# Performance work log

Measured on AMD Instinct MI355X. Metric: run time of the kernel, lower is better.

The kernel has to match this reference:

```python
import jax, jax.numpy as jnp
import numpy as np

B, SECL, WORDL = 16, 8, 512
S = SECL * WORDL
H, E, V, NOOV = 256, 128, 50000, 32
EOS = 3
FSIZE = 2  # config.mode == 'train'


def setup_inputs() -> dict:
    key = jax.random.key(0)
    ks = jax.random.split(key, 24)
    g = lambda i, shape, s=0.02: jax.random.normal(ks[i], shape, jnp.float32) * s
    inp = jax.random.randint(ks[0], (B,), 0, V)
    inp = inp.at[:4].set(EOS)  # exercise focus-update branch
    h = g(1, (B, H), 0.1)
    c = g(2, (B, H), 0.1)
    enc_outputs = g(3, (B, S, 2 * H), 1.0)
    enc_feature = g(4, (B, S, 2 * H), 0.1)
    enc_sec_output = g(5, (B, SECL, 2 * H), 1.0)
    enc_mask = jnp.ones((B, S), jnp.float32)
    sec_mask = jnp.ones((B, SECL), jnp.float32)
    prev_context = g(6, (B, 2 * H), 0.1)
    zeros_oov = jnp.zeros((B, NOOV), jnp.float32)
    enc_input_oov = jax.random.randint(ks[7], (B, S), 0, V + NOOV)
    coverage = jnp.zeros((B, S), jnp.float32)
    # sparse nonneg focus distribution over sections (guaranteed >=1 nonzero/row)
    u = jax.random.uniform(ks[8], (B, SECL))
    f = u * (u > 0.5)
    fb = jax.nn.one_hot(jnp.argmax(u, axis=1), SECL)
    f = jnp.where(f.sum(1, keepdims=True) > 0, f, fb)
    focus = f / f.sum(1, keepdims=True)
    params = dict(
        embedding=g(9, (V, E)),
        W_comb=g(10, (E, 2 * H + E)), b_comb=jnp.zeros((E,), jnp.float32),
        W_ih=g(11, (4 * H, E)), W_hh=g(12, (4 * H, H)),
        b_ih=jnp.zeros((4 * H,), jnp.float32), b_hh=jnp.zeros((4 * H,), jnp.float32),
        W_d=g(13, (2 * H, 2 * H)), b_d=jnp.zeros((2 * H,), jnp.float32),
        W_feat=g(14, (2 * H, 2 * H)), v_sec=g(15, (2 * H,)),
        W_dec=g(16, (2 * H, 2 * H)), b_dec=jnp.zeros((2 * H,), jnp.float32),
        w_cov=g(17, (2 * H,)), v_att=g(18, (2 * H,)),
        W_pgen=g(19, (1, 4 * H + E)), b_pgen=jnp.zeros((1,), jnp.float32),
        W_out=g(20, (V, 3 * H)), b_out=g(21, (V,)),
    )
    return dict(inp=inp, h=h, c=c, enc_outputs=enc_outputs, enc_feature=enc_feature,
                enc_sec_output=enc_sec_output, enc_mask=enc_mask, sec_mask=sec_mask,
                prev_context=prev_context, zeros_oov=zeros_oov, enc_input_oov=enc_input_oov,
                coverage=coverage, focus=focus, **params)


def _focus_update(focus, sad):
    # rem_mask: positions from the first nonzero of focus onward
    fz = jnp.cumprod((focus == 0).astype(sad.dtype), axis=1)
    rem_mask = (fz == 0).astype(sad.dtype)
    focus_index = jnp.sum(fz, axis=1).astype(jnp.int32)  # index of first nonzero
    focus_mask = jax.nn.one_hot(focus_index, SECL, dtype=sad.dtype)
    rem_ex = rem_mask - focus_mask
    focus_beta = sad * focus_mask
    rem_beta = sad * rem_ex
    max_rem_beta = rem_beta.max(axis=1)
    max_rem_ind = jnp.argmax(rem_beta, axis=1)
    compare = (focus_beta.max(axis=1) * 2 > max_rem_beta).astype(sad.dtype)[:, None]
    # train branch
    src = (max_rem_beta != 0).astype(sad.dtype)[:, None]
    max_rem_mask = jax.nn.one_hot(max_rem_ind, SECL, dtype=sad.dtype) * src
    cp2 = jnp.cumprod((max_rem_mask == 0).astype(sad.dtype), axis=1)
    after = (cp2 == 0).astype(sad.dtype) - max_rem_mask
    amb = sad * after
    mam_mask = (jax.nn.one_hot(jnp.argmax(amb, axis=1), SECL, dtype=sad.dtype)
                * (amb.max(axis=1) != 0).astype(sad.dtype)[:, None])
    case_f = focus_beta + sad * max_rem_mask
    case_r = sad * (max_rem_mask + mam_mask)
    fu = compare * case_f + (1 - compare) * case_r
    return fu / fu.sum(1, keepdims=True)


def reference(inp, h, c, enc_outputs, enc_feature, enc_sec_output, enc_mask, sec_mask,
              prev_context, zeros_oov, enc_input_oov, coverage, focus,
              embedding, W_comb, b_comb, W_ih, W_hh, b_ih, b_hh,
              W_d, b_d, W_feat, v_sec, W_dec, b_dec, w_cov, v_att,
              W_pgen, b_pgen, W_out, b_out):
    inp_is_eos = (inp == EOS).astype(jnp.float32)[:, None]  # [B,1] -> bcast over secL
    emb = embedding[inp]  # [B,E]
    x = jnp.concatenate([prev_context, emb], axis=1) @ W_comb.T + b_comb  # [B,E]
    # single LSTM step (torch gate order i,f,g,o)
    gates = x @ W_ih.T + b_ih + h @ W_hh.T + b_hh
    gi_, gf_, gg_, go_ = jnp.split(gates, 4, axis=1)
    c_new = jax.nn.sigmoid(gf_) * c + jax.nn.sigmoid(gi_) * jnp.tanh(gg_)
    h_new = jax.nn.sigmoid(go_) * jnp.tanh(c_new)
    dec_state = jnp.concatenate([h_new, c_new], axis=1)  # [B,2H]
    # section attention
    feat = enc_sec_output @ W_feat.T  # [B,secL,2H]
    d = dec_state @ W_d.T + b_d
    sc = jnp.tanh(feat + d[:, None, :]) @ v_sec  # [B,secL]
    sad = jax.nn.softmax(sc, axis=1) * sec_mask
    sad = sad / sad.sum(1, keepdims=True)
    # hard-attention focus update (only where input was EOS)
    fu = _focus_update(focus, sad)
    focus = inp_is_eos * fu + (1 - inp_is_eos) * focus
    # word attention with coverage
    dfeat = dec_state @ W_dec.T + b_dec
    att = enc_feature + dfeat[:, None, :] + coverage[:, :, None] * w_cov[None, None, :]
    score = jnp.tanh(att) @ v_att  # [B,S]
    score3 = score.reshape(B, SECL, WORDL)
    topk_focus, gidx = jax.lax.top_k(focus, FSIZE)  # [B,FSIZE]
    bidx = jnp.arange(B)[:, None]
    score_g = score3[bidx, gidx].reshape(B, FSIZE * WORDL)
    mask_g = enc_mask.reshape(B, SECL, WORDL)[bidx, gidx].reshape(B, FSIZE * WORDL)
    af = jax.nn.softmax(score_g, axis=1) * mask_g
    af = af / af.sum(1, keepdims=True)
    af = topk_focus[:, :, None] * af.reshape(B, FSIZE, WORDL)
    attn = jnp.zeros((B, SECL, WORDL), af.dtype).at[bidx, gidx].set(af).reshape(B, S)
    attn = attn / attn.sum(1, keepdims=True)
    context = jnp.einsum('bs,bsd->bd', attn, enc_outputs)  # [B,2H]
    coverage = coverage + attn
    # pointer-generator
    p_gen = jax.nn.sigmoid(jnp.concatenate([context, dec_state, x], axis=1) @ W_pgen.T + b_pgen)
    logits = jnp.concatenate([h_new, context], axis=1) @ W_out.T + b_out
    vocab_dist = jax.nn.softmax(logits, axis=1)
    vext = jnp.concatenate([p_gen * vocab_dist, zeros_oov], axis=1)  # [B,V+NOOV]
    final = vext.at[bidx, enc_input_oov].add((1 - p_gen) * attn)
    return final, h_new, c_new, context, attn, coverage, focus, sad
```

## Files before the change

kernel.cpp:

```cpp
#include <hip/hip_runtime.h>
#include <math.h>

#define NB 16
#define SECL 8
#define WORDL 512
#define SS 4096
#define HH 256
#define EE 128
#define VV 50000
#define NOOV 32
#define VO 50032
#define EOS_ID 3
#define H2 512
#define KOUT 768
#define NCH 13
#define CHSZ 4096

#define OFF_FINAL 0
#define OFF_H    800512
#define OFF_C    804608
#define OFF_CTX  808704
#define OFF_ATTN 816896
#define OFF_COV  882432
#define OFF_FOC  947968
#define OFF_SAD  948096

#define WX     0
#define WD     2048
#define WDF    10240
#define WSC    18432
#define WGI    18560
#define WTF    18592
#define WSG    18624
#define WPART  35008
#define WPG    166080
#define WPM    166096
#define WPS    166304
#define WLG    166512

__device__ __forceinline__ float sigm(float x){ return 1.f/(1.f+__expf(-x)); }
__device__ __forceinline__ float tfast(float x){
  float ax = fabsf(x);
  float e  = __expf(-2.f*ax);
  float t  = (1.f-e)/(1.f+e);
  return x < 0.f ? -t : t;
}
__device__ __forceinline__ float dot4(float acc, float4 a, float4 b){
  acc = fmaf(a.x,b.x,acc); acc = fmaf(a.y,b.y,acc);
  acc = fmaf(a.z,b.z,acc); acc = fmaf(a.w,b.w,acc);
  return acc;
}
__device__ __forceinline__ float dot2(float acc, float2 a, float2 b){
  acc = fmaf(a.x,b.x,acc); acc = fmaf(a.y,b.y,acc);
  return acc;
}
__device__ __forceinline__ float mergep(float a, float b, int k, int lane){
  float send = (lane & k) ? a : b;
  float recv = __shfl_xor(send, k);
  return (lane & k) ? b + recv : a + recv;
}
__device__ __forceinline__ float reduce8(float acc[8], int lane){
  float m0 = mergep(acc[0], acc[1], 1, lane);
  float m1 = mergep(acc[2], acc[3], 1, lane);
  float m2 = mergep(acc[4], acc[5], 1, lane);
  float m3 = mergep(acc[6], acc[7], 1, lane);
  float n0 = mergep(m0, m1, 2, lane);
  float n1 = mergep(m2, m3, 2, lane);
  float p  = mergep(n0, n1, 4, lane);
  p += __shfl_xor(p, 8);
  p += __shfl_xor(p, 16);
  p += __shfl_xor(p, 32);
  return p;
}


__global__ void __launch_bounds__(256)
k_x(const int* __restrict__ inp, const float* __restrict__ pc,
    const float* __restrict__ emb, const float* __restrict__ Wc,
    const float* __restrict__ bc, float* __restrict__ ws){
  int lane = threadIdx.x & 63;
  int gw = blockIdx.x*4 + (threadIdx.x >> 6);
  int bg = gw & 1, e = gw >> 1;
  float4 z = {0,0,0,0};
  float4 i0[8], i1[8], i2[8];
  #pragma unroll
  for(int j=0;j<8;j++){
    int b = bg*8 + j;
    i0[j] = *(const float4*)(pc + b*H2 + lane*4);
    i1[j] = *(const float4*)(pc + b*H2 + 256 + lane*4);
    i2[j] = (lane < 32) ? *(const float4*)(emb + (size_t)inp[b]*EE + lane*4) : z;
  }
  const float* wr = Wc + (size_t)e*(H2+EE);
  float4 w0 = *(const float4*)(wr + lane*4);
  float4 w1 = *(const float4*)(wr + 256 + lane*4);
  float4 w2 = (lane < 32) ? *(const float4*)(wr + 512 + lane*4) : z;
  float acc[8];
  #pragma unroll
  for(int j=0;j<8;j++){
    float a = dot4(0.f, w0, i0[j]);
    a = dot4(a, w1, i1[j]);
    a = dot4(a, w2, i2[j]);
    acc[j] = a;
  }
  float p = reduce8(acc, lane);
  if(lane < 8) ws[WX + (bg*8+lane)*EE + e] = p + bc[e];
}

__global__ void __launch_bounds__(256)
k_gates(const float* __restrict__ h, const float* __restrict__ c,
        const float* __restrict__ Wih, const float* __restrict__ Whh,
        const float* __restrict__ bih, const float* __restrict__ bhh,
        const float* __restrict__ ws, float* __restrict__ out){
  __shared__ float g_lds[4][8];
  int lane = threadIdx.x & 63;
  int wv   = threadIdx.x >> 6;
  int j  = blockIdx.x >> 1;
  int bg = blockIdx.x & 1;
  float2 xb[8]; float4 hb[8];
  #pragma unroll
  for(int q=0;q<8;q++){
    int b = bg*8 + q;
    xb[q] = *(const float2*)(ws + WX + b*EE + lane*2);
    hb[q] = *(const float4*)(h + b*HH + lane*4);
  }
  int r = wv*HH + j;
  float2 wx = *(const float2*)(Wih + (size_t)r*EE + lane*2);
  float4 wh = *(const float4*)(Whh + (size_t)r*HH + lane*4);
  float acc[8];
  #pragma unroll
  for(int q=0;q<8;q++)
    acc[q] = dot4(dot2(0.f, wx, xb[q]), wh, hb[q]);
  float p = reduce8(acc, lane);
  if(lane < 8) g_lds[wv][lane] = p + bih[r] + bhh[r];
  __syncthreads();
  if(threadIdx.x < 8){
    int b = bg*8 + threadIdx.x;
    float g0 = g_lds[0][threadIdx.x], g1 = g_lds[1][threadIdx.x];
    float g2 = g_lds[2][threadIdx.x], g3 = g_lds[3][threadIdx.x];
    float cn = sigm(g1)*c[b*HH + j] + sigm(g0)*tfast(g2);
    float hn = sigm(g3)*tfast(cn);
    out[OFF_H + b*HH + j] = hn;
    out[OFF_C + b*HH + j] = cn;
  }
}

__global__ void __launch_bounds__(256)
k_dd(const float* __restrict__ Wd, const float* __restrict__ bd,
     const float* __restrict__ Wdec, const float* __restrict__ bdec,
     const float* __restrict__ out, float* __restrict__ ws){
  int lane = threadIdx.x & 63;
  int gw = blockIdx.x*4 + (threadIdx.x >> 6);
  int bg = gw & 1, sel = (gw >> 1) & 1, j = gw >> 2;
  float4 d0[8], d1[8];
  #pragma unroll
  for(int q=0;q<8;q++){
    int b = bg*8 + q;
    d0[q] = *(const float4*)(out + OFF_H + b*HH + lane*4);
    d1[q] = *(const float4*)(out + OFF_C + b*HH + lane*4);
  }
  const float* wr = (sel ? Wdec : Wd) + (size_t)j*H2;
  float4 w0 = *(const float4*)(wr + lane*4);
  float4 w1 = *(const float4*)(wr + 256 + lane*4);
  float acc[8];
  #pragma unroll
  for(int q=0;q<8;q++)
    acc[q] = dot4(dot4(0.f, w0, d0[q]), w1, d1[q]);
  float p = reduce8(acc, lane);
  if(lane < 8) ws[(sel ? WDF : WD) + (bg*8+lane)*H2 + j] = p + (sel ? bdec : bd)[j];
}

__global__ void __launch_bounds__(256)
k_sec(const float* __restrict__ eso, const float* __restrict__ Wf,
      const float* __restrict__ vsec, float* __restrict__ ws){
  __shared__ float red[4];
  int lane = threadIdx.x & 63;
  int wv   = threadIdx.x >> 6;
  int bl = blockIdx.x; int b = bl >> 3;
  const float* ep = eso + (size_t)bl*H2;
  float4 es0 = *(const float4*)(ep + lane*4);
  float4 es1 = *(const float4*)(ep + 256 + lane*4);
  const float* dp = ws + WD + b*H2;
  float local = 0.f;
  for(int t=0;t<16;t++){
    int j0 = wv*8 + t*32;
    float acc[8];
    #pragma unroll
    for(int jj=0;jj<8;jj++){
      const float* wr = Wf + (size_t)(j0+jj)*H2;
      float4 w0 = *(const float4*)(wr + lane*4);
      float4 w1 = *(const float4*)(wr + 256 + lane*4);
      acc[jj] = dot4(dot4(0.f, w0, es0), w1, es1);
    }
    float p = reduce8(acc, lane);
    if(lane < 8){
      int j = j0 + lane;
      local += tfast(p + dp[j]) * vsec[j];
    }
  }
  local += __shfl_xor(local, 1);
  local += __shfl_xor(local, 2);
  local += __shfl_xor(local, 4);
  if(lane == 0) red[wv] = local;
  __syncthreads();
  if(threadIdx.x == 0) ws[WSC + bl] = red[0]+red[1]+red[2]+red[3];
}

__global__ void k_focus(const int* __restrict__ inp, const float* __restrict__ smask,
                        const float* __restrict__ focus_in, float* __restrict__ ws,
                        float* __restrict__ out){
  int b = threadIdx.x;
  if(b >= NB) return;
  float sc[SECL], sad[SECL], f[SECL];
  float mx = -1e30f;
  for(int l=0;l<SECL;l++){ sc[l] = ws[WSC + b*SECL + l]; mx = fmaxf(mx, sc[l]); }
  float sum = 0.f;
  for(int l=0;l<SECL;l++){ sad[l] = __expf(sc[l]-mx); sum += sad[l]; }
  float s2 = 0.f;
  for(int l=0;l<SECL;l++){ sad[l] = sad[l]/sum * smask[b*SECL+l]; s2 += sad[l]; }
  for(int l=0;l<SECL;l++){ sad[l] /= s2; out[OFF_SAD + b*SECL + l] = sad[l]; }
  for(int l=0;l<SECL;l++) f[l] = focus_in[b*SECL+l];
  int fi = SECL;
  for(int l=0;l<SECL;l++){ if(f[l] != 0.f){ fi = l; break; } }
  float rem[SECL];
  for(int l=0;l<SECL;l++) rem[l] = (l > fi) ? sad[l] : 0.f;
  float mrb = rem[0]; int mri = 0;
  for(int l=1;l<SECL;l++){ if(rem[l] > mrb){ mrb = rem[l]; mri = l; } }
  float fbm = (fi < SECL) ? sad[fi] : 0.f;
  int cmp = (fbm*2.f > mrb);
  int src = (mrb != 0.f);
  float amb[SECL];
  for(int l=0;l<SECL;l++) amb[l] = (src && l > mri) ? sad[l] : 0.f;
  float am = amb[0]; int ai = 0;
  for(int l=1;l<SECL;l++){ if(amb[l] > am){ am = amb[l]; ai = l; } }
  float fu[SECL]; float fs = 0.f;
  for(int l=0;l<SECL;l++){
    float mrm = (src && l == mri) ? 1.f : 0.f;
    float mam = ((am != 0.f) && l == ai) ? 1.f : 0.f;
    float cf = ((l==fi) ? sad[l] : 0.f) + sad[l]*mrm;
    float cr = sad[l]*(mrm + mam);
    fu[l] = cmp ? cf : cr;
    fs += fu[l];
  }
  float eos = (inp[b] == EOS_ID) ? 1.f : 0.f;
  float fo[SECL];
  for(int l=0;l<SECL;l++){
    fo[l] = eos*(fu[l]/fs) + (1.f-eos)*f[l];
    out[OFF_FOC + b*SECL + l] = fo[l];
  }
  float v1 = fo[0]; int i1 = 0;
  for(int l=1;l<SECL;l++){ if(fo[l] > v1){ v1 = fo[l]; i1 = l; } }
  float v2 = -1e30f; int i2 = 0;
  for(int l=0;l<SECL;l++){ if(l != i1 && fo[l] > v2){ v2 = fo[l]; i2 = l; } }
  ((int*)ws)[WGI + b*2]     = i1;
  ((int*)ws)[WGI + b*2 + 1] = i2;
  ws[WTF + b*2]     = v1;
  ws[WTF + b*2 + 1] = v2;
}


__global__ void k_score(const float* __restrict__ ef, const float* __restrict__ cov,
                        const float* __restrict__ wcov, const float* __restrict__ vatt,
                        float* __restrict__ ws){
  int lane = threadIdx.x & 63;
  int o = blockIdx.x*4 + (threadIdx.x >> 6);
  int b = o >> 10, fidx = (o >> 9) & 1, w = o & 511;
  int g = ((const int*)ws)[WGI + b*2 + fidx];
  int s = g*WORDL + w;
  const float* e  = ef + ((size_t)(b*SS + s))*H2;
  const float* df = ws + WDF + b*H2;
  float cv = cov[b*SS + s];
  int j = lane*4;
  float local = 0.f;
  #pragma unroll
  for(int half=0; half<2; half++){
    int jj = j + half*256;
    float4 a  = *(const float4*)(e+jj);
    float4 d4 = *(const float4*)(df+jj);
    float4 wc = *(const float4*)(wcov+jj);
    float4 va = *(const float4*)(vatt+jj);
    local += tfast(a.x + d4.x + cv*wc.x)*va.x;
    local += tfast(a.y + d4.y + cv*wc.y)*va.y;
    local += tfast(a.z + d4.z + cv*wc.z)*va.z;
    local += tfast(a.w + d4.w + cv*wc.w)*va.w;
  }
  for(int off=32; off>0; off>>=1) local += __shfl_xor(local, off);
  if(lane == 0) ws[WSG + o] = local;
}

__global__ void k_af(const float* __restrict__ emask, const float* __restrict__ cov,
                     float* __restrict__ ws, float* __restrict__ out){
  __shared__ float es[1024];
  __shared__ float red[256];
  int b = blockIdx.x, tid = threadIdx.x;
  int g0 = ((int*)ws)[WGI+b*2], g1 = ((int*)ws)[WGI+b*2+1];
  float tf0 = ws[WTF+b*2], tf1 = ws[WTF+b*2+1];
  float lm = -1e30f;
  for(int i=tid;i<1024;i+=256) lm = fmaxf(lm, ws[WSG + b*1024 + i]);
  red[tid] = lm; __syncthreads();
  for(int off=128; off; off>>=1){
    if(tid < off) red[tid] = fmaxf(red[tid], red[tid+off]);
    __syncthreads();
  }
  float mx = red[0]; __syncthreads();
  float ls0 = 0.f, ls1 = 0.f;
  for(int i=tid;i<1024;i+=256){
    int fidx = i >> 9, w = i & 511;
    int g = fidx ? g1 : g0;
    float m = emask[b*SS + g*WORDL + w];
    float ev = __expf(ws[WSG + b*1024 + i] - mx)*m;
    es[i] = ev;
    if(fidx) ls1 += ev; else ls0 += ev;
  }
  red[tid] = ls0; __syncthreads();
  for(int off=128; off; off>>=1){ if(tid<off) red[tid]+=red[tid+off]; __syncthreads(); }
  float sum0 = red[0]; __syncthreads();
  red[tid] = ls1; __syncthreads();
  for(int off=128; off; off>>=1){ if(tid<off) red[tid]+=red[tid+off]; __syncthreads(); }
  float sum1 = red[0]; __syncthreads();
  float inv = 1.f/(tf0*sum0 + tf1*sum1);
  for(int s=tid;s<SS;s+=256){
    int sec = s >> 9, w = s & 511;
    float a = 0.f;
    if(sec == g0)      a = tf0*es[w]*inv;
    else if(sec == g1) a = tf1*es[512+w]*inv;
    out[OFF_ATTN + b*SS + s] = a;
    out[OFF_COV  + b*SS + s] = cov[b*SS+s] + a;
  }
}

__global__ void k_ctxp(const float* __restrict__ eo, const float* __restrict__ out,
                       float* __restrict__ ws){
  int blk = blockIdx.x; int b = blk >> 4, ch = blk & 15;
  int d = threadIdx.x;
  int g0 = ((const int*)ws)[WGI + b*2];
  int g1 = ((const int*)ws)[WGI + b*2 + 1];
  float a0 = 0.f, a1 = 0.f;
  #pragma unroll 4
  for(int p = ch*64; p < ch*64 + 64; p++){
    int s = ((p >> 9) ? g1 : g0)*WORDL + (p & 511);
    float a = out[OFF_ATTN + b*SS + s];
    const float* ep = eo + ((size_t)(b*SS + s))*H2;
    a0 = fmaf(a, ep[d],       a0);
    a1 = fmaf(a, ep[d+256],   a1);
  }
  ws[WPART + (size_t)blk*H2 + d]       = a0;
  ws[WPART + (size_t)blk*H2 + d + 256] = a1;
}

__global__ void k_ctx(const float* __restrict__ Wp, const float* __restrict__ bp,
                      float* __restrict__ ws, float* __restrict__ out){
  __shared__ float red[256];
  int b = blockIdx.x, tid = threadIdx.x;
  float c0 = 0.f, c1 = 0.f;
  for(int ch=0; ch<16; ch++){
    c0 += ws[WPART + (size_t)(b*16+ch)*H2 + tid];
    c1 += ws[WPART + (size_t)(b*16+ch)*H2 + tid + 256];
  }
  out[OFF_CTX + b*H2 + tid]       = c0;
  out[OFF_CTX + b*H2 + tid + 256] = c1;
  float hn = out[OFF_H + b*HH + tid];
  float cn = out[OFF_C + b*HH + tid];
  float pv = c0*Wp[tid] + c1*Wp[tid+256] + hn*Wp[512+tid] + cn*Wp[768+tid];
  if(tid < EE) pv = fmaf(ws[WX + b*EE + tid], Wp[1024+tid], pv);
  red[tid] = pv; __syncthreads();
  for(int off=128; off; off>>=1){ if(tid<off) red[tid]+=red[tid+off]; __syncthreads(); }
  if(tid == 0) ws[WPG + b] = sigm(red[0] + bp[0]);
}

#define LG_NBLK  768
#define LG_STRIDE (LG_NBLK*2)
#define LG_ITERS 33
__global__ void __launch_bounds__(256,3)
k_logits(const float* __restrict__ Wout, const float* __restrict__ bout,
         const float* __restrict__ out, float* __restrict__ ws){
  int lane = threadIdx.x & 63;
  int wv   = threadIdx.x >> 6;
  int bg   = wv & 1;
  int rh   = wv >> 1;
  float4 hb0[8], hb1[8], hb2[8];
  #pragma unroll
  for(int j=0;j<8;j++){
    int b = bg*8 + j;
    hb0[j] = *(const float4*)(out + OFF_H   + b*HH + lane*4);
    hb1[j] = *(const float4*)(out + OFF_CTX + b*H2 + lane*4);
    hb2[j] = *(const float4*)(out + OFF_CTX + b*H2 + 256 + lane*4);
  }
  int vbase = blockIdx.x*2 + rh;
  const float* p0 = Wout + (size_t)vbase*KOUT + lane*4;
  float4 A0 = *(const float4*)(p0);
  float4 A1 = *(const float4*)(p0+256);
  float4 A2 = *(const float4*)(p0+512);
  int v1c = vbase + LG_STRIDE; if(v1c >= VV) v1c = VV-1;
  const float* p1 = Wout + (size_t)v1c*KOUT + lane*4;
  float4 B0 = *(const float4*)(p1);
  float4 B1 = *(const float4*)(p1+256);
  float4 B2 = *(const float4*)(p1+512);
  for(int j=0;j<LG_ITERS;j++){
    int v = vbase + j*LG_STRIDE;
    float4 C0=B0, C1=B1, C2=B2;
    if(j < LG_ITERS-2){
      int vn = v + 2*LG_STRIDE; if(vn >= VV) vn = VV-1;
      const float* np = Wout + (size_t)vn*KOUT + lane*4;
      C0 = *(const float4*)(np);
      C1 = *(const float4*)(np+256);
      C2 = *(const float4*)(np+512);
    }
    float acc[8];
    #pragma unroll
    for(int q=0;q<8;q++){
      float a = dot4(0.f, A0, hb0[q]);
      a = dot4(a, A1, hb1[q]);
      a = dot4(a, A2, hb2[q]);
      acc[q] = a;
    }
    float p = reduce8(acc, lane);
    if(v < VV && lane < 8)
      ws[WLG + (size_t)(bg*8+lane)*VV + v] = p + bout[v];
    A0=B0; A1=B1; A2=B2;
    B0=C0; B1=C1; B2=C2;
  }
}


__global__ void k_vms(float* __restrict__ ws){
  __shared__ float rm[256], rs[256];
  int blk = blockIdx.x; int b = blk/NCH, ch = blk%NCH;
  int tid = threadIdx.x;
  int v0 = ch*CHSZ; int v1 = v0+CHSZ; if(v1 > VV) v1 = VV;
  float mt = -1e30f, st = 0.f;
  for(int v=v0+tid; v<v1; v+=256){
    float x = ws[WLG + (size_t)b*VV + v];
    if(x > mt){ st = st*__expf(mt - x) + 1.f; mt = x; }
    else       st += __expf(x - mt);
  }
  rm[tid] = mt; rs[tid] = st; __syncthreads();
  for(int off=128; off; off>>=1){
    if(tid < off){
      float ma = rm[tid], mb = rm[tid+off];
      float M = fmaxf(ma, mb);
      rs[tid] = rs[tid]*__expf(ma-M) + rs[tid+off]*__expf(mb-M);
      rm[tid] = M;
    }
    __syncthreads();
  }
  if(tid == 0){ ws[WPM + blk] = rm[0]; ws[WPS + blk] = rs[0]; }
}

__global__ void k_final(const float* __restrict__ zoov, float* __restrict__ ws,
                        float* __restrict__ out){
  int blk = blockIdx.x; int b = blk/NCH, ch = blk%NCH;
  float mx = -1e30f, sm = 0.f;
  for(int i=0;i<NCH;i++){ mx = fmaxf(mx, ws[WPM + b*NCH + i]); }
  for(int i=0;i<NCH;i++){ sm += ws[WPS + b*NCH + i]*__expf(ws[WPM + b*NCH + i] - mx); }
  float scale = ws[WPG + b] / sm;
  int v0 = ch*CHSZ; int v1 = v0+CHSZ; if(v1 > VO) v1 = VO;
  for(int v=v0+threadIdx.x; v<v1; v+=256){
    float r;
    if(v < VV) r = scale*__expf(ws[WLG + (size_t)b*VV + v] - mx);
    else       r = zoov[b*NOOV + v - VV];
    out[OFF_FINAL + (size_t)b*VO + v] = r;
  }
}

__global__ void k_scatter(const int* __restrict__ oov, const float* __restrict__ ws,
                          float* __restrict__ out){
  int blk = blockIdx.x; int b = blk >> 4;
  int s = (blk & 15)*256 + threadIdx.x;
  float a = out[OFF_ATTN + b*SS + s];
  if(a != 0.f){
    float w = (1.f - ws[WPG + b])*a;
    atomicAdd(out + OFF_FINAL + (size_t)b*VO + oov[b*SS + s], w);
  }
}

extern "C" void kernel_launch(void* const* d_in, const int* in_sizes, int n_in,
                              void* d_out, int out_size, void* d_ws, size_t ws_size,
                              hipStream_t stream){
  const int*   inp   = (const int*)  d_in[0];
  const float* h     = (const float*)d_in[1];
  const float* c     = (const float*)d_in[2];
  const float* eo    = (const float*)d_in[3];
  const float* efeat = (const float*)d_in[4];
  const float* eso   = (const float*)d_in[5];
  const float* emask = (const float*)d_in[6];
  const float* smask = (const float*)d_in[7];
  const float* pctx  = (const float*)d_in[8];
  const float* zoov  = (const float*)d_in[9];
  const int*   oov   = (const int*)  d_in[10];
  const float* cov   = (const float*)d_in[11];
  const float* foc   = (const float*)d_in[12];
  const float* emb   = (const float*)d_in[13];
  const float* Wc    = (const float*)d_in[14];
  const float* bc    = (const float*)d_in[15];
  const float* Wih   = (const float*)d_in[16];
  const float* Whh   = (const float*)d_in[17];
  const float* bih   = (const float*)d_in[18];
  const float* bhh   = (const float*)d_in[19];
  const float* Wd    = (const float*)d_in[20];
  const float* bd    = (const float*)d_in[21];
  const float* Wf    = (const float*)d_in[22];
  const float* vsec  = (const float*)d_in[23];
  const float* Wdec  = (const float*)d_in[24];
  const float* bdec  = (const float*)d_in[25];
  const float* wcov  = (const float*)d_in[26];
  const float* vatt  = (const float*)d_in[27];
  const float* Wp    = (const float*)d_in[28];
  const float* bp    = (const float*)d_in[29];
  const float* Wout  = (const float*)d_in[30];
  const float* bout  = (const float*)d_in[31];
  float* out = (float*)d_out;
  float* ws  = (float*)d_ws;

  k_x      <<<64,      256, 0, stream>>>(inp, pctx, emb, Wc, bc, ws);
  k_gates  <<<512,     256, 0, stream>>>(h, c, Wih, Whh, bih, bhh, ws, out);
  k_dd     <<<512,     256, 0, stream>>>(Wd, bd, Wdec, bdec, out, ws);
  k_sec    <<<128,     256, 0, stream>>>(eso, Wf, vsec, ws);
  k_focus  <<<1,        64, 0, stream>>>(inp, smask, foc, ws, out);
  k_score  <<<4096,    256, 0, stream>>>(efeat, cov, wcov, vatt, ws);
  k_af     <<<16,      256, 0, stream>>>(emask, cov, ws, out);
  k_ctxp   <<<256,     256, 0, stream>>>(eo, out, ws);
  k_ctx    <<<16,      256, 0, stream>>>(Wp, bp, ws, out);
  k_logits <<<LG_NBLK, 256, 0, stream>>>(Wout, bout, out, ws);
  k_vms    <<<208,     256, 0, stream>>>(ws);
  k_final  <<<208,     256, 0, stream>>>(zoov, ws, out);
  k_scatter<<<256,     256, 0, stream>>>(oov, ws, out);
}
```

Measured before the change: 131.1 us.

## Fuse focus into score, merge softmax/final/scatter, and tile logits rows contiguously

```diff
diff --git a/kernel.cpp b/kernel.cpp
--- a/kernel.cpp
+++ b/kernel.cpp
@@ -13,8 +13,6 @@
 #define EOS_ID 3
 #define H2 512
 #define KOUT 768
-#define NCH 13
-#define CHSZ 4096
 
 #define OFF_FINAL 0
 #define OFF_H    800512
@@ -34,8 +32,6 @@
 #define WSG    18624
 #define WPART  35008
 #define WPG    166080
-#define WPM    166096
-#define WPS    166304
 #define WLG    166512
 
 __device__ __forceinline__ float sigm(float x){ return 1.f/(1.f+__expf(-x)); }
@@ -71,6 +67,50 @@
   p += __shfl_xor(p, 16);
   p += __shfl_xor(p, 32);
   return p;
+}
+
+__device__ __forceinline__ void focus_compute(int b, const float sc[SECL],
+    const int* inp, const float* smask, const float* focus_in,
+    float fo[SECL], float sad[SECL], int* pi1, int* pi2, float* pv1, float* pv2){
+  float f[SECL];
+  float mx = -1e30f;
+  for(int l=0;l<SECL;l++) mx = fmaxf(mx, sc[l]);
+  float sum = 0.f;
+  for(int l=0;l<SECL;l++){ sad[l] = __expf(sc[l]-mx); sum += sad[l]; }
+  float s2 = 0.f;
+  for(int l=0;l<SECL;l++){ sad[l] = sad[l]/sum * smask[b*SECL+l]; s2 += sad[l]; }
+  for(int l=0;l<SECL;l++) sad[l] /= s2;
+  for(int l=0;l<SECL;l++) f[l] = focus_in[b*SECL+l];
+  int fi = SECL;
+  for(int l=0;l<SECL;l++){ if(f[l] != 0.f){ fi = l; break; } }
+  float rem[SECL];
+  for(int l=0;l<SECL;l++) rem[l] = (l > fi) ? sad[l] : 0.f;
+  float mrb = rem[0]; int mri = 0;
+  for(int l=1;l<SECL;l++){ if(rem[l] > mrb){ mrb = rem[l]; mri = l; } }
+  float fbm = (fi < SECL) ? sad[fi] : 0.f;
+  int cmp = (fbm*2.f > mrb);
+  int src = (mrb != 0.f);
+  float amb[SECL];
+  for(int l=0;l<SECL;l++) amb[l] = (src && l > mri) ? sad[l] : 0.f;
+  float am = amb[0]; int ai = 0;
+  for(int l=1;l<SECL;l++){ if(amb[l] > am){ am = amb[l]; ai = l; } }
+  float fu[SECL]; float fs = 0.f;
+  for(int l=0;l<SECL;l++){
+    float mrm = (src && l == mri) ? 1.f : 0.f;
+    float mam = ((am != 0.f) && l == ai) ? 1.f : 0.f;
+    float cf = ((l==fi) ? sad[l] : 0.f) + sad[l]*mrm;
+    float cr = sad[l]*(mrm + mam);
+    fu[l] = cmp ? cf : cr;
+    fs += fu[l];
+  }
+  float eos = (inp[b] == EOS_ID) ? 1.f : 0.f;
+  for(int l=0;l<SECL;l++)
+    fo[l] = eos*(fu[l]/fs) + (1.f-eos)*f[l];
+  float v1 = fo[0]; int i1 = 0;
+  for(int l=1;l<SECL;l++){ if(fo[l] > v1){ v1 = fo[l]; i1 = l; } }
+  float v2 = -1e30f; int i2 = 0;
+  for(int l=0;l<SECL;l++){ if(l != i1 && fo[l] > v2){ v2 = fo[l]; i2 = l; } }
+  *pi1 = i1; *pi2 = i2; *pv1 = v1; *pv2 = v2;
 }
 
 
@@ -205,66 +245,39 @@
   if(threadIdx.x == 0) ws[WSC + bl] = red[0]+red[1]+red[2]+red[3];
 }
 
-__global__ void k_focus(const int* __restrict__ inp, const float* __restrict__ smask,
-                        const float* __restrict__ focus_in, float* __restrict__ ws,
-                        float* __restrict__ out){
-  int b = threadIdx.x;
-  if(b >= NB) return;
-  float sc[SECL], sad[SECL], f[SECL];
-  float mx = -1e30f;
-  for(int l=0;l<SECL;l++){ sc[l] = ws[WSC + b*SECL + l]; mx = fmaxf(mx, sc[l]); }
-  float sum = 0.f;
-  for(int l=0;l<SECL;l++){ sad[l] = __expf(sc[l]-mx); sum += sad[l]; }
-  float s2 = 0.f;
-  for(int l=0;l<SECL;l++){ sad[l] = sad[l]/sum * smask[b*SECL+l]; s2 += sad[l]; }
-  for(int l=0;l<SECL;l++){ sad[l] /= s2; out[OFF_SAD + b*SECL + l] = sad[l]; }
-  for(int l=0;l<SECL;l++) f[l] = focus_in[b*SECL+l];
-  int fi = SECL;
-  for(int l=0;l<SECL;l++){ if(f[l] != 0.f){ fi = l; break; } }
-  float rem[SECL];
-  for(int l=0;l<SECL;l++) rem[l] = (l > fi) ? sad[l] : 0.f;
-  float mrb = rem[0]; int mri = 0;
-  for(int l=1;l<SECL;l++){ if(rem[l] > mrb){ mrb = rem[l]; mri = l; } }
-  float fbm = (fi < SECL) ? sad[fi] : 0.f;
-  int cmp = (fbm*2.f > mrb);
-  int src = (mrb != 0.f);
-  float amb[SECL];
-  for(int l=0;l<SECL;l++) amb[l] = (src && l > mri) ? sad[l] : 0.f;
-  float am = amb[0]; int ai = 0;
-  for(int l=1;l<SECL;l++){ if(amb[l] > am){ am = amb[l]; ai = l; } }
-  float fu[SECL]; float fs = 0.f;
-  for(int l=0;l<SECL;l++){
-    float mrm = (src && l == mri) ? 1.f : 0.f;
-    float mam = ((am != 0.f) && l == ai) ? 1.f : 0.f;
-    float cf = ((l==fi) ? sad[l] : 0.f) + sad[l]*mrm;
-    float cr = sad[l]*(mrm + mam);
-    fu[l] = cmp ? cf : cr;
-    fs += fu[l];
-  }
-  float eos = (inp[b] == EOS_ID) ? 1.f : 0.f;
-  float fo[SECL];
-  for(int l=0;l<SECL;l++){
-    fo[l] = eos*(fu[l]/fs) + (1.f-eos)*f[l];
-    out[OFF_FOC + b*SECL + l] = fo[l];
-  }
-  float v1 = fo[0]; int i1 = 0;
-  for(int l=1;l<SECL;l++){ if(fo[l] > v1){ v1 = fo[l]; i1 = l; } }
-  float v2 = -1e30f; int i2 = 0;
-  for(int l=0;l<SECL;l++){ if(l != i1 && fo[l] > v2){ v2 = fo[l]; i2 = l; } }
-  ((int*)ws)[WGI + b*2]     = i1;
-  ((int*)ws)[WGI + b*2 + 1] = i2;
-  ws[WTF + b*2]     = v1;
-  ws[WTF + b*2 + 1] = v2;
-}
-
-
-__global__ void k_score(const float* __restrict__ ef, const float* __restrict__ cov,
-                        const float* __restrict__ wcov, const float* __restrict__ vatt,
-                        float* __restrict__ ws){
-  int lane = threadIdx.x & 63;
-  int o = blockIdx.x*4 + (threadIdx.x >> 6);
+__global__ void __launch_bounds__(256)
+k_score(const float* __restrict__ ef, const float* __restrict__ cov,
+        const float* __restrict__ wcov, const float* __restrict__ vatt,
+        const int* __restrict__ inp, const float* __restrict__ smask,
+        const float* __restrict__ foc,
+        float* __restrict__ ws, float* __restrict__ out){
+  __shared__ int   gi_l[NB*2];
+  __shared__ float tf_l[NB*2];
+  int tid = threadIdx.x;
+  if(tid < NB){
+    int b = tid;
+    float sc[SECL];
+    for(int l=0;l<SECL;l++) sc[l] = ws[WSC + b*SECL + l];
+    float fo[SECL], sad[SECL]; int i1,i2; float v1,v2;
+    focus_compute(b, sc, inp, smask, foc, fo, sad, &i1, &i2, &v1, &v2);
+    gi_l[b*2] = i1; gi_l[b*2+1] = i2;
+    tf_l[b*2] = v1; tf_l[b*2+1] = v2;
+    if(blockIdx.x == 0){
+      for(int l=0;l<SECL;l++){
+        out[OFF_SAD + b*SECL + l] = sad[l];
+        out[OFF_FOC + b*SECL + l] = fo[l];
+      }
+      ((int*)ws)[WGI + b*2]     = i1;
+      ((int*)ws)[WGI + b*2 + 1] = i2;
+      ws[WTF + b*2]     = v1;
+      ws[WTF + b*2 + 1] = v2;
+    }
+  }
+  __syncthreads();
+  int lane = tid & 63;
+  int o = blockIdx.x*4 + (tid >> 6);
   int b = o >> 10, fidx = (o >> 9) & 1, w = o & 511;
-  int g = ((const int*)ws)[WGI + b*2 + fidx];
+  int g = gi_l[b*2 + fidx];
   int s = g*WORDL + w;
   const float* e  = ef + ((size_t)(b*SS + s))*H2;
   const float* df = ws + WDF + b*H2;
@@ -367,9 +380,10 @@
   if(tid == 0) ws[WPG + b] = sigm(red[0] + bp[0]);
 }
 
-#define LG_NBLK  768
-#define LG_STRIDE (LG_NBLK*2)
-#define LG_ITERS 33
+#define LG_NBLK 768
+#define LG_ROWS 16
+#define LG_WIN  (LG_NBLK*LG_ROWS)
+#define LG_NWIN 5
 __global__ void __launch_bounds__(256,3)
 k_logits(const float* __restrict__ Wout, const float* __restrict__ bout,
          const float* __restrict__ out, float* __restrict__ ws){
@@ -385,56 +399,60 @@
     hb1[j] = *(const float4*)(out + OFF_CTX + b*H2 + lane*4);
     hb2[j] = *(const float4*)(out + OFF_CTX + b*H2 + 256 + lane*4);
   }
-  int vbase = blockIdx.x*2 + rh;
-  const float* p0 = Wout + (size_t)vbase*KOUT + lane*4;
-  float4 A0 = *(const float4*)(p0);
-  float4 A1 = *(const float4*)(p0+256);
-  float4 A2 = *(const float4*)(p0+512);
-  int v1c = vbase + LG_STRIDE; if(v1c >= VV) v1c = VV-1;
-  const float* p1 = Wout + (size_t)v1c*KOUT + lane*4;
-  float4 B0 = *(const float4*)(p1);
-  float4 B1 = *(const float4*)(p1+256);
-  float4 B2 = *(const float4*)(p1+512);
-  for(int j=0;j<LG_ITERS;j++){
-    int v = vbase + j*LG_STRIDE;
-    float4 C0=B0, C1=B1, C2=B2;
-    if(j < LG_ITERS-2){
-      int vn = v + 2*LG_STRIDE; if(vn >= VV) vn = VV-1;
-      const float* np = Wout + (size_t)vn*KOUT + lane*4;
-      C0 = *(const float4*)(np);
-      C1 = *(const float4*)(np+256);
-      C2 = *(const float4*)(np+512);
+  for(int w=0; w<LG_NWIN; w++){
+    int v0 = w*LG_WIN + blockIdx.x*LG_ROWS + rh*8;
+    if(v0 >= VV) break;
+    int va = v0;
+    const float* pa = Wout + (size_t)va*KOUT + lane*4;
+    float4 A0 = *(const float4*)(pa);
+    float4 A1 = *(const float4*)(pa+256);
+    float4 A2 = *(const float4*)(pa+512);
+    int vb = v0+1; int vbc = vb < VV ? vb : VV-1;
+    const float* pb = Wout + (size_t)vbc*KOUT + lane*4;
+    float4 B0 = *(const float4*)(pb);
+    float4 B1 = *(const float4*)(pb+256);
+    float4 B2 = *(const float4*)(pb+512);
+    #pragma unroll
+    for(int r=0;r<8;r++){
+      int v = v0 + r;
+      float4 C0=B0, C1=B1, C2=B2;
+      if(r < 6){
+        int vn = v0 + r + 2; int vnc = vn < VV ? vn : VV-1;
+        const float* np = Wout + (size_t)vnc*KOUT + lane*4;
+        C0 = *(const float4*)(np);
+        C1 = *(const float4*)(np+256);
+        C2 = *(const float4*)(np+512);
+      }
+      float acc[8];
+      #pragma unroll
+      for(int q=0;q<8;q++){
+        float a = dot4(0.f, A0, hb0[q]);
+        a = dot4(a, A1, hb1[q]);
+        a = dot4(a, A2, hb2[q]);
+        acc[q] = a;
+      }
+      float p = reduce8(acc, lane);
+      if(v < VV && lane < 8)
+        ws[WLG + (size_t)(bg*8+lane)*VV + v] = p + bout[v];
+      A0=B0; A1=B1; A2=B2;
+      B0=C0; B1=C1; B2=C2;
     }
-    float acc[8];
-    #pragma unroll
-    for(int q=0;q<8;q++){
-      float a = dot4(0.f, A0, hb0[q]);
-      a = dot4(a, A1, hb1[q]);
-      a = dot4(a, A2, hb2[q]);
-      acc[q] = a;
-    }
-    float p = reduce8(acc, lane);
-    if(v < VV && lane < 8)
-      ws[WLG + (size_t)(bg*8+lane)*VV + v] = p + bout[v];
-    A0=B0; A1=B1; A2=B2;
-    B0=C0; B1=C1; B2=C2;
-  }
-}
-
-
-__global__ void k_vms(float* __restrict__ ws){
-  __shared__ float rm[256], rs[256];
-  int blk = blockIdx.x; int b = blk/NCH, ch = blk%NCH;
-  int tid = threadIdx.x;
-  int v0 = ch*CHSZ; int v1 = v0+CHSZ; if(v1 > VV) v1 = VV;
+  }
+}
+
+__global__ void __launch_bounds__(1024)
+k_out(const float* __restrict__ zoov, const int* __restrict__ oov,
+      float* __restrict__ ws, float* __restrict__ out){
+  __shared__ float rm[1024], rs[1024];
+  int b = blockIdx.x, tid = threadIdx.x;
   float mt = -1e30f, st = 0.f;
-  for(int v=v0+tid; v<v1; v+=256){
+  for(int v=tid; v<VV; v+=1024){
     float x = ws[WLG + (size_t)b*VV + v];
     if(x > mt){ st = st*__expf(mt - x) + 1.f; mt = x; }
     else       st += __expf(x - mt);
   }
   rm[tid] = mt; rs[tid] = st; __syncthreads();
-  for(int off=128; off; off>>=1){
+  for(int off=512; off; off>>=1){
     if(tid < off){
       float ma = rm[tid], mb = rm[tid+off];
       float M = fmaxf(ma, mb);
@@ -443,34 +461,21 @@
     }
     __syncthreads();
   }
-  if(tid == 0){ ws[WPM + blk] = rm[0]; ws[WPS + blk] = rs[0]; }
-}
-
-__global__ void k_final(const float* __restrict__ zoov, float* __restrict__ ws,
-                        float* __restrict__ out){
-  int blk = blockIdx.x; int b = blk/NCH, ch = blk%NCH;
-  float mx = -1e30f, sm = 0.f;
-  for(int i=0;i<NCH;i++){ mx = fmaxf(mx, ws[WPM + b*NCH + i]); }
-  for(int i=0;i<NCH;i++){ sm += ws[WPS + b*NCH + i]*__expf(ws[WPM + b*NCH + i] - mx); }
-  float scale = ws[WPG + b] / sm;
-  int v0 = ch*CHSZ; int v1 = v0+CHSZ; if(v1 > VO) v1 = VO;
-  for(int v=v0+threadIdx.x; v<v1; v+=256){
-    float r;
-    if(v < VV) r = scale*__expf(ws[WLG + (size_t)b*VV + v] - mx);
-    else       r = zoov[b*NOOV + v - VV];
+  float mx = rm[0], sm = rs[0];
+  float pg = ws[WPG + b];
+  float scale = pg / sm;
+  for(int v=tid; v<VO; v+=1024){
+    float r = (v < VV) ? scale*__expf(ws[WLG + (size_t)b*VV + v] - mx)
+                       : zoov[b*NOOV + v - VV];
     out[OFF_FINAL + (size_t)b*VO + v] = r;
   }
-}
-
-__global__ void k_scatter(const int* __restrict__ oov, const float* __restrict__ ws,
-                          float* __restrict__ out){
-  int blk = blockIdx.x; int b = blk >> 4;
-  int s = (blk & 15)*256 + threadIdx.x;
+  __syncthreads();
+  int fidx = tid >> 9, w = tid & 511;
+  int g = ((const int*)ws)[WGI + b*2 + fidx];
+  int s = g*WORDL + w;
   float a = out[OFF_ATTN + b*SS + s];
-  if(a != 0.f){
-    float w = (1.f - ws[WPG + b])*a;
-    atomicAdd(out + OFF_FINAL + (size_t)b*VO + oov[b*SS + s], w);
-  }
+  if(a != 0.f)
+    atomicAdd(out + OFF_FINAL + (size_t)b*VO + oov[b*SS + s], (1.f - pg)*a);
 }
 
 extern "C" void kernel_launch(void* const* d_in, const int* in_sizes, int n_in,
@@ -511,17 +516,14 @@
   float* out = (float*)d_out;
   float* ws  = (float*)d_ws;
 
-  k_x      <<<64,      256, 0, stream>>>(inp, pctx, emb, Wc, bc, ws);
-  k_gates  <<<512,     256, 0, stream>>>(h, c, Wih, Whh, bih, bhh, ws, out);
-  k_dd     <<<512,     256, 0, stream>>>(Wd, bd, Wdec, bdec, out, ws);
-  k_sec    <<<128,     256, 0, stream>>>(eso, Wf, vsec, ws);
-  k_focus  <<<1,        64, 0, stream>>>(inp, smask, foc, ws, out);
-  k_score  <<<4096,    256, 0, stream>>>(efeat, cov, wcov, vatt, ws);
-  k_af     <<<16,      256, 0, stream>>>(emask, cov, ws, out);
-  k_ctxp   <<<256,     256, 0, stream>>>(eo, out, ws);
-  k_ctx    <<<16,      256, 0, stream>>>(Wp, bp, ws, out);
-  k_logits <<<LG_NBLK, 256, 0, stream>>>(Wout, bout, out, ws);
-  k_vms    <<<208,     256, 0, stream>>>(ws);
-  k_final  <<<208,     256, 0, stream>>>(zoov, ws, out);
-  k_scatter<<<256,     256, 0, stream>>>(oov, ws, out);
-}
+  k_x      <<<64,      256,  0, stream>>>(inp, pctx, emb, Wc, bc, ws);
+  k_gates  <<<512,     256,  0, stream>>>(h, c, Wih, Whh, bih, bhh, ws, out);
+  k_dd     <<<512,     256,  0, stream>>>(Wd, bd, Wdec, bdec, out, ws);
+  k_sec    <<<128,     256,  0, stream>>>(eso, Wf, vsec, ws);
+  k_score  <<<4096,    256,  0, stream>>>(efeat, cov, wcov, vatt, inp, smask, foc, ws, out);
+  k_af     <<<16,      256,  0, stream>>>(emask, cov, ws, out);
+  k_ctxp   <<<256,     256,  0, stream>>>(eo, out, ws);
+  k_ctx    <<<16,      256,  0, stream>>>(Wp, bp, ws, out);
+  k_logits <<<LG_NBLK, 256,  0, stream>>>(Wout, bout, out, ws);
+  k_out    <<<16,      1024, 0, stream>>>(zoov, oov, ws, out);
+}
```

Measured after the change: 153.7 us. 1.17x slower.
